# Optimization experiments

Hardware: AMD Instinct MI355X
Metric: run time of the kernel (lower is better)

## Reference

```python
import jax, jax.numpy as jnp
import numpy as np

BIT = 8
QMAX = 2 ** (BIT - 1) - 1          # 127
QMIN = -(2 ** (BIT - 1))           # -128
BOUNDARY_RANGE = 0.005
EPS = 1e-5


def _quant_act_int8(x):
    # StatsQ per-tensor activation quantization: scale from (1 - boundary_range)
    # quantile of |x| (robust absmax), fake-quant with STE.
    amax = jnp.maximum(jnp.quantile(jnp.abs(x), 1.0 - BOUNDARY_RANGE), EPS)
    s = QMAX / amax
    q = jnp.clip(jnp.round(x * s), QMIN, QMAX) / s
    return x + jax.lax.stop_gradient(q - x)


def _quant_w_ternary(w):
    # BitNet-1.58-style per-tensor ternary weight quantization:
    # gamma = mean(|W|); W_q in {-1, 0, +1} * gamma; STE.
    gamma = jnp.mean(jnp.abs(w)) + EPS
    q = jnp.clip(jnp.round(w / gamma), -1.0, 1.0) * gamma
    return w + jax.lax.stop_gradient(q - w)


def _qlinear(x, w):
    # quantize activations (int8 fake-quant) and weights (ternary), then matmul
    xq = _quant_act_int8(x)
    wq = _quant_w_ternary(w)
    return jnp.einsum('btd,hd->bth', xq, wq)


def _layernorm(x, g, b):
    mu = jnp.mean(x, axis=-1, keepdims=True)
    var = jnp.mean(jnp.square(x - mu), axis=-1, keepdims=True)
    return (x - mu) * jax.lax.rsqrt(var + 1e-5) * g + b


def setup_inputs() -> dict:
    key = jax.random.key(0)
    k_x, k_w1, k_w2 = jax.random.split(key, 3)
    B, T, D, H = 64, 256, 1024, 4096
    x = jax.random.normal(k_x, (B, T, D), dtype=jnp.float32)
    ln_g = jnp.ones((D,), dtype=jnp.float32)
    ln_b = jnp.zeros((D,), dtype=jnp.float32)
    w1 = jax.random.normal(k_w1, (H, D), dtype=jnp.float32) * (1.0 / np.sqrt(D))
    w2 = jax.random.normal(k_w2, (D, H), dtype=jnp.float32) * (1.0 / np.sqrt(H))
    return {'x': x, 'ln_g': ln_g, 'ln_b': ln_b, 'w1': w1, 'w2': w2}


def reference(x, ln_g, ln_b, w1, w2):
    h = _layernorm(x, ln_g, ln_b)          # [B,T,D]
    h = _qlinear(h, w1)                    # [B,T,H]
    h = jax.nn.gelu(h, approximate=False)  # torch nn.GELU default = exact erf
    out = _qlinear(h, w2)                  # [B,T,D]
    return out
```

## Files before the change

### kernel.cpp

```cpp
#include <hip/hip_runtime.h>
#include <hip/hip_fp16.h>
#include <math.h>


#define M_ROWS 16384
#define D_DIM  1024
#define H_DIM  4096

typedef int i32x4 __attribute__((ext_vector_type(4)));
typedef int i32x16 __attribute__((ext_vector_type(16)));

#define AS1 __attribute__((address_space(1)))
#define AS3 __attribute__((address_space(3)))

__device__ __forceinline__ void load_lds16(const void* g, void* l) {
  __builtin_amdgcn_global_load_lds((const AS1 void*)g, (AS3 void*)l, 16, 0, 0);
}

__device__ __forceinline__ float block_sum256(float v, float* lds) {
#pragma unroll
  for (int o = 32; o > 0; o >>= 1) v += __shfl_down(v, o, 64);
  int t = threadIdx.x;
  __syncthreads();
  if ((t & 63) == 0) lds[t >> 6] = v;
  __syncthreads();
  return lds[0] + lds[1] + lds[2] + lds[3];
}

__global__ __launch_bounds__(256) void k_layernorm(
    const float* __restrict__ x, const float* __restrict__ g,
    const float* __restrict__ b, __half* __restrict__ out) {
  __shared__ float lds[4];
  int row = blockIdx.x, t = threadIdx.x;
  float4 v = ((const float4*)(x + (size_t)row * D_DIM))[t];
  float s = v.x + v.y + v.z + v.w;
  s = block_sum256(s, lds);
  float mu = s * (1.0f / D_DIM);
  float d0 = v.x - mu, d1 = v.y - mu, d2 = v.z - mu, d3 = v.w - mu;
  float ss = d0 * d0 + d1 * d1 + d2 * d2 + d3 * d3;
  ss = block_sum256(ss, lds);
  float inv = 1.0f / sqrtf(ss * (1.0f / D_DIM) + 1e-5f);
  float4 gg = ((const float4*)g)[t];
  float4 bb = ((const float4*)b)[t];
  __half2 p0 = __floats2half2_rn(d0 * inv * gg.x + bb.x, d1 * inv * gg.y + bb.y);
  __half2 p1 = __floats2half2_rn(d2 * inv * gg.z + bb.z, d3 * inv * gg.w + bb.w);
  uint2 st;
  st.x = *(unsigned*)&p0;
  st.y = *(unsigned*)&p1;
  ((uint2*)(out + (size_t)row * D_DIM))[t] = st;
}

__global__ __launch_bounds__(256) void k_absmean2(const float4* __restrict__ w1,
                                                  const float4* __restrict__ w2,
                                                  size_t n4, double* __restrict__ out) {
  int which = (blockIdx.x >= (gridDim.x >> 1)) ? 1 : 0;
  const float4* p = which ? w2 : w1;
  unsigned half_grid = gridDim.x >> 1;
  unsigned blk = blockIdx.x - which * half_grid;
  double s = 0.0;
  size_t stride = (size_t)half_grid * blockDim.x;
  for (size_t i = (size_t)blk * blockDim.x + threadIdx.x; i < n4; i += stride) {
    float4 v = p[i];
    s += (double)fabsf(v.x) + (double)fabsf(v.y) + (double)fabsf(v.z) + (double)fabsf(v.w);
  }
#pragma unroll
  for (int o = 32; o > 0; o >>= 1) s += __shfl_down(s, o, 64);
  __shared__ double ds[4];
  int t = threadIdx.x;
  if ((t & 63) == 0) ds[t >> 6] = s;
  __syncthreads();
  if (t == 0) atomicAdd(out + which, ds[0] + ds[1] + ds[2] + ds[3]);
}

__device__ __forceinline__ int tern1(float w, float gamma) {
  return (int)fminf(1.f, fmaxf(-1.f, rintf(w / gamma)));
}

__global__ __launch_bounds__(256) void k_wquant2(const float4* __restrict__ w1,
                                                 const float4* __restrict__ w2,
                                                 unsigned* __restrict__ q1,
                                                 unsigned* __restrict__ q2, size_t n4,
                                                 const double* __restrict__ sump,
                                                 double inv_n, float* __restrict__ gamma_out) {
  int which = (blockIdx.x >= (gridDim.x >> 1)) ? 1 : 0;
  const float4* w = which ? w2 : w1;
  unsigned* wq = which ? q2 : q1;
  unsigned half_grid = gridDim.x >> 1;
  unsigned blk = blockIdx.x - which * half_grid;
  float gamma = (float)(sump[which] * inv_n) + 1e-5f;
  if (blk == 0 && threadIdx.x == 0) gamma_out[which] = gamma;
  size_t stride = (size_t)half_grid * blockDim.x;
  for (size_t i = (size_t)blk * blockDim.x + threadIdx.x; i < n4; i += stride) {
    float4 v = w[i];
    int a = tern1(v.x, gamma), b = tern1(v.y, gamma), c = tern1(v.z, gamma), d = tern1(v.w, gamma);
    wq[i] = (unsigned)(a & 255) | ((unsigned)(b & 255) << 8) |
            ((unsigned)(c & 255) << 16) | ((unsigned)(d & 255) << 24);
  }
}

__global__ __launch_bounds__(512) void k_hist16(const uint4* __restrict__ p, size_t n8,
                                                unsigned* __restrict__ hist) {
  extern __shared__ unsigned h[];
  int t = threadIdx.x;
  for (int i = t; i < 32768; i += 512) h[i] = 0;
  __syncthreads();
  size_t stride = (size_t)gridDim.x * 512;
  for (size_t i = (size_t)blockIdx.x * 512 + t; i < n8; i += stride) {
    uint4 u = p[i];
    atomicAdd(&h[u.x & 0x7FFFu], 1u);
    atomicAdd(&h[(u.x >> 16) & 0x7FFFu], 1u);
    atomicAdd(&h[u.y & 0x7FFFu], 1u);
    atomicAdd(&h[(u.y >> 16) & 0x7FFFu], 1u);
    atomicAdd(&h[u.z & 0x7FFFu], 1u);
    atomicAdd(&h[(u.z >> 16) & 0x7FFFu], 1u);
    atomicAdd(&h[u.w & 0x7FFFu], 1u);
    atomicAdd(&h[(u.w >> 16) & 0x7FFFu], 1u);
  }
  __syncthreads();
  for (int i = t; i < 32768; i += 512) {
    unsigned c = h[i];
    if (c) atomicAdd(&hist[i], c);
  }
}

__global__ __launch_bounds__(256) void k_scanq(const unsigned* __restrict__ hist,
                                               float* __restrict__ scl,
                                               unsigned long long k, double frac) {
  __shared__ unsigned tsum[256];
  __shared__ unsigned long long pre[256];
  __shared__ unsigned vk, vk1;
  int t = threadIdx.x;
  unsigned s = 0;
  for (int j = 0; j < 128; ++j) s += hist[t * 128 + j];
  tsum[t] = s;
  __syncthreads();
  if (t == 0) {
    unsigned long long c = 0;
    for (int i = 0; i < 256; ++i) { pre[i] = c; c += tsum[i]; }
  }
  __syncthreads();
  unsigned long long base = pre[t];
  for (int j = 0; j < 128; ++j) {
    unsigned c = hist[t * 128 + j];
    if (base <= k && k < base + c) vk = t * 128 + j;
    if (base <= k + 1 && k + 1 < base + c) vk1 = t * 128 + j;
    base += c;
  }
  __syncthreads();
  if (t == 0) {
    double a = (double)__half2float(__ushort_as_half((unsigned short)vk));
    double b = (double)__half2float(__ushort_as_half((unsigned short)vk1));
    double qv = (frac >= 0.5) ? (b - (b - a) * (1.0 - frac)) : (a + (b - a) * frac);
    float amax = fmaxf((float)qv, 1e-5f);
    scl[0] = amax;
    scl[1] = 127.0f / amax;
  }
}

__device__ __forceinline__ void unpack8(uint4 u, float* f) {
  __half2 h;
  h = *(__half2*)&u.x; f[0] = __low2float(h); f[1] = __high2float(h);
  h = *(__half2*)&u.y; f[2] = __low2float(h); f[3] = __high2float(h);
  h = *(__half2*)&u.z; f[4] = __low2float(h); f[5] = __high2float(h);
  h = *(__half2*)&u.w; f[6] = __low2float(h); f[7] = __high2float(h);
}

__device__ __forceinline__ unsigned qpack4(float a, float b, float c, float d, float s) {
  int qa = (int)fminf(127.f, fmaxf(-128.f, rintf(a * s)));
  int qb = (int)fminf(127.f, fmaxf(-128.f, rintf(b * s)));
  int qc = (int)fminf(127.f, fmaxf(-128.f, rintf(c * s)));
  int qd = (int)fminf(127.f, fmaxf(-128.f, rintf(d * s)));
  return (unsigned)(qa & 255) | ((unsigned)(qb & 255) << 8) |
         ((unsigned)(qc & 255) << 16) | ((unsigned)(qd & 255) << 24);
}

__global__ __launch_bounds__(256) void k_quant16(const uint4* __restrict__ p,
                                                 uint2* __restrict__ q, size_t n8,
                                                 const float* __restrict__ scl) {
  float s = scl[1];
  size_t stride = (size_t)gridDim.x * blockDim.x;
  for (size_t i = (size_t)blockIdx.x * blockDim.x + threadIdx.x; i < n8; i += stride) {
    float f[8];
    unpack8(p[i], f);
    uint2 r;
    r.x = qpack4(f[0], f[1], f[2], f[3], s);
    r.y = qpack4(f[4], f[5], f[6], f[7], s);
    q[i] = r;
  }
}

__device__ __forceinline__ float gelu_fast(float v) {
  float a = fabsf(v) * 0.70710678118654752f;
  float t = __builtin_amdgcn_rcpf(fmaf(0.3275911f, a, 1.0f));
  float p = t * fmaf(t, fmaf(t, fmaf(t, fmaf(t, 1.061405429f, -1.453152027f),
                                     1.421413741f), -0.284496736f), 0.254829592f);
  float e = __expf(-a * a);
  float er = fmaf(-p, e, 1.0f);
  float erf_s = copysignf(er, v);
  return 0.5f * v * (1.0f + erf_s);
}

template <int K, bool GELU>
__global__ __launch_bounds__(512, 2) void k_gemm(const signed char* __restrict__ A,
                                                 const signed char* __restrict__ B,
                                                 int N, void* __restrict__ outp,
                                                 const float* __restrict__ gamma_p,
                                                 const float* __restrict__ scl) {
  constexpr int NT = K / 128;
  extern __shared__ __align__(16) char smem[];
  signed char* As = (signed char*)smem;
  signed char* Bs = (signed char*)smem + 65536;

  const int tid = threadIdx.x;
  const int lane = tid & 63;
  const int wv = tid >> 6;
  const int wr = (wv >> 2) * 128;
  const int wc = (wv & 3) * 64;

  const unsigned nwg = gridDim.x;
  const unsigned q8 = nwg >> 3;
  const unsigned bid = blockIdx.x;
  const unsigned swz = (bid & 7) * q8 + (bid >> 3);
  const unsigned nx = (unsigned)N >> 8;
  const int n0 = (int)(swz % nx) * 256;
  const int m0 = (int)(swz / nx) * 256;

  const signed char* aG[4];
  const signed char* bG[4];
  int sL[4];
#pragma unroll
  for (int j = 0; j < 4; ++j) {
    int g_lin = j * 512 + tid;
    int row = g_lin >> 3;
    int cg = (g_lin & 7) ^ (row & 7);
    aG[j] = A + (size_t)(m0 + row) * K + cg * 16;
    bG[j] = B + (size_t)(n0 + row) * K + cg * 16;
    sL[j] = g_lin * 16;
  }

#define STAGE(t_)                                              \
  {                                                            \
    const size_t ko_ = (size_t)(t_) * 128;                     \
    const int bo_ = ((t_) & 1) << 15;                          \
    _Pragma("unroll") for (int j = 0; j < 4; ++j)              \
        load_lds16(aG[j] + ko_, As + bo_ + sL[j]);             \
    _Pragma("unroll") for (int j = 0; j < 4; ++j)              \
        load_lds16(bG[j] + ko_, Bs + bo_ + sL[j]);             \
  }

  int a_off[4][4], b_off[2][4];
#pragma unroll
  for (int mi = 0; mi < 4; ++mi) {
    int am = wr + mi * 32 + (lane & 31);
#pragma unroll
    for (int p = 0; p < 4; ++p) {
      int g = p * 2 + (lane >> 5);
      a_off[mi][p] = am * 128 + ((g ^ (am & 7)) << 4);
    }
  }
#pragma unroll
  for (int ni = 0; ni < 2; ++ni) {
    int bn = wc + ni * 32 + (lane & 31);
#pragma unroll
    for (int p = 0; p < 4; ++p) {
      int g = p * 2 + (lane >> 5);
      b_off[ni][p] = bn * 128 + ((g ^ (bn & 7)) << 4);
    }
  }

#define RD(fa, fb, bo_, p_)                                      \
  {                                                              \
    _Pragma("unroll") for (int mi = 0; mi < 4; ++mi)             \
        fa[mi] = *(const i32x4*)(As + (bo_) + a_off[mi][p_]);    \
    _Pragma("unroll") for (int ni = 0; ni < 2; ++ni)             \
        fb[ni] = *(const i32x4*)(Bs + (bo_) + b_off[ni][p_]);    \
  }

#define MM(fa, fb)                                                            \
  {                                                                           \
    __builtin_amdgcn_s_setprio(1);                                            \
    _Pragma("unroll") for (int mi = 0; mi < 4; ++mi)                          \
        _Pragma("unroll") for (int ni = 0; ni < 2; ++ni)                      \
            acc[mi][ni] = __builtin_amdgcn_mfma_i32_32x32x32_i8(              \
                fa[mi], fb[ni], acc[mi][ni], 0, 0, 0);                        \
    __builtin_amdgcn_s_setprio(0);                                            \
  }

  i32x16 acc[4][2];
#pragma unroll
  for (int mi = 0; mi < 4; ++mi)
#pragma unroll
    for (int ni = 0; ni < 2; ++ni) acc[mi][ni] = (i32x16)(0);

  i32x4 fA0[4], fB0[2], fA1[4], fB1[2];

  STAGE(0);
  STAGE(1);
  asm volatile("s_waitcnt vmcnt(8)" ::: "memory");
  __builtin_amdgcn_s_barrier();
  RD(fA0, fB0, 0, 0);

#pragma unroll 2
  for (int t = 0; t < NT; ++t) {
    const int bo = (t & 1) << 15;
    if (t >= 1 && t + 1 < NT) STAGE(t + 1);
    RD(fA1, fB1, bo, 1);
    __builtin_amdgcn_sched_barrier(0);
    MM(fA0, fB0);
    __builtin_amdgcn_sched_barrier(0);
    RD(fA0, fB0, bo, 2);
    __builtin_amdgcn_sched_barrier(0);
    MM(fA1, fB1);
    __builtin_amdgcn_sched_barrier(0);
    RD(fA1, fB1, bo, 3);
    __builtin_amdgcn_sched_barrier(0);
    MM(fA0, fB0);
    __builtin_amdgcn_sched_barrier(0);
    MM(fA1, fB1);
    if (t + 1 < NT) {
      asm volatile("s_waitcnt vmcnt(0)" ::: "memory");
      __builtin_amdgcn_s_barrier();
      RD(fA0, fB0, bo ^ 32768, 0);
    }
  }
#undef STAGE
#undef RD
#undef MM

  const float cs = (*gamma_p) / scl[1];
  const int col0 = n0 + wc + (lane & 31);
  const int row0 = m0 + wr + 4 * (lane >> 5);
#pragma unroll
  for (int mi = 0; mi < 4; ++mi) {
#pragma unroll
    for (int ni = 0; ni < 2; ++ni) {
      const int col = col0 + ni * 32;
#pragma unroll
      for (int reg = 0; reg < 16; ++reg) {
        const int row = row0 + mi * 32 + (reg & 3) + 8 * (reg >> 2);
        float v = cs * (float)acc[mi][ni][reg];
        size_t idx = (size_t)row * N + col;
        if (GELU) {
          ((__half*)outp)[idx] = __float2half(gelu_fast(v));
        } else {
          ((float*)outp)[idx] = v;
        }
      }
    }
  }
}

extern "C" void kernel_launch(void* const* d_in, const int* in_sizes, int n_in,
                              void* d_out, int out_size, void* d_ws, size_t ws_size,
                              hipStream_t stream) {
  const float* x = (const float*)d_in[0];
  const float* ln_g = (const float*)d_in[1];
  const float* ln_b = (const float*)d_in[2];
  const float* w1 = (const float*)d_in[3];
  const float* w2 = (const float*)d_in[4];
  float* out = (float*)d_out;

  char* ws = (char*)d_ws;
  __half* h2 = (__half*)ws;
  __half* h1 = (__half*)(ws + ((size_t)128 << 20));
  signed char* xq1 = (signed char*)(ws + ((size_t)160 << 20));
  signed char* xq2 = (signed char*)(ws + ((size_t)128 << 20));
  signed char* w1q = (signed char*)(ws + ((size_t)192 << 20));
  signed char* w2q = (signed char*)(ws + ((size_t)196 << 20));
  char* sm = ws + ((size_t)200 << 20);
  unsigned* hista = (unsigned*)sm;
  unsigned* histb = (unsigned*)(sm + (128 << 10));
  double* wsum = (double*)(sm + (256 << 10));
  float* gamma = (float*)(sm + (256 << 10) + 16);
  float* scl1 = (float*)(sm + (256 << 10) + 32);
  float* scl2 = (float*)(sm + (256 << 10) + 40);

  hipMemsetAsync(sm, 0, (256 << 10) + 64, stream);
  hipFuncSetAttribute((const void*)k_hist16, hipFuncAttributeMaxDynamicSharedMemorySize,
                      131072);
  hipFuncSetAttribute((const void*)(k_gemm<D_DIM, true>),
                      hipFuncAttributeMaxDynamicSharedMemorySize, 131072);
  hipFuncSetAttribute((const void*)(k_gemm<H_DIM, false>),
                      hipFuncAttributeMaxDynamicSharedMemorySize, 131072);

  const double qq = 1.0 - 0.005;
  const unsigned long long N1 = (unsigned long long)M_ROWS * D_DIM;
  const unsigned long long N2 = (unsigned long long)M_ROWS * H_DIM;
  double idx1 = qq * (double)(N1 - 1);
  double idx2 = qq * (double)(N2 - 1);
  unsigned long long k1 = (unsigned long long)idx1;
  unsigned long long k2 = (unsigned long long)idx2;
  double frac1 = idx1 - (double)k1;
  double frac2 = idx2 - (double)k2;

  const size_t nW4 = (size_t)H_DIM * D_DIM / 4;
  const double inv_nW = 1.0 / (double)(H_DIM * D_DIM);

  k_absmean2<<<1024, 256, 0, stream>>>((const float4*)w1, (const float4*)w2, nW4, wsum);
  k_wquant2<<<2048, 256, 0, stream>>>((const float4*)w1, (const float4*)w2,
                                      (unsigned*)w1q, (unsigned*)w2q, nW4, wsum, inv_nW, gamma);

  k_layernorm<<<M_ROWS, 256, 0, stream>>>(x, ln_g, ln_b, h1);

  const size_t n8_1 = N1 / 8;
  k_hist16<<<256, 512, 131072, stream>>>((const uint4*)h1, n8_1, hista);
  k_scanq<<<1, 256, 0, stream>>>(hista, scl1, k1, frac1);
  k_quant16<<<1024, 256, 0, stream>>>((const uint4*)h1, (uint2*)xq1, n8_1, scl1);

  k_gemm<D_DIM, true><<<(H_DIM / 256) * (M_ROWS / 256), 512, 131072, stream>>>(
      xq1, w1q, H_DIM, (void*)h2, gamma + 0, scl1);

  const size_t n8_2 = N2 / 8;
  k_hist16<<<256, 512, 131072, stream>>>((const uint4*)h2, n8_2, histb);
  k_scanq<<<1, 256, 0, stream>>>(histb, scl2, k2, frac2);
  k_quant16<<<2048, 256, 0, stream>>>((const uint4*)h2, (uint2*)xq2, n8_2, scl2);

  k_gemm<H_DIM, false><<<(D_DIM / 256) * (M_ROWS / 256), 512, 131072, stream>>>(
      xq2, w2q, D_DIM, (void*)out, gamma + 1, scl2);
}
```

Measured before the change: 468.2 us.

## Stage GEMM tiles through registers instead of direct global-to-LDS loads

Replaces the direct global_load_lds staging with ordinary global loads into registers, issued two iterations ahead and written to the double-buffered LDS after the compute phases. The explicit fragment ping-pong between LDS reads and MFMA groups is dropped in favour of four simple phases that each read and then multiply. The aim is to overlap global latency with a full tile of MFMA work and to simplify scheduling. The cost is extra VGPRs for the staged tiles, an added barrier per iteration, and less explicit interleaving of LDS reads with MFMAs.

```diff
diff --git a/kernel.cpp b/kernel.cpp
--- a/kernel.cpp
+++ b/kernel.cpp
@@ -9,13 +9,6 @@
 
 typedef int i32x4 __attribute__((ext_vector_type(4)));
 typedef int i32x16 __attribute__((ext_vector_type(16)));
-
-#define AS1 __attribute__((address_space(1)))
-#define AS3 __attribute__((address_space(3)))
-
-__device__ __forceinline__ void load_lds16(const void* g, void* l) {
-  __builtin_amdgcn_global_load_lds((const AS1 void*)g, (AS3 void*)l, 16, 0, 0);
-}
 
 __device__ __forceinline__ float block_sum256(float v, float* lds) {
 #pragma unroll
@@ -225,27 +218,36 @@
   const int n0 = (int)(swz % nx) * 256;
   const int m0 = (int)(swz / nx) * 256;
 
-  const signed char* aG[4];
-  const signed char* bG[4];
-  int sL[4];
+  int aOff[4], bOff[4], sL[4];
 #pragma unroll
   for (int j = 0; j < 4; ++j) {
     int g_lin = j * 512 + tid;
     int row = g_lin >> 3;
     int cg = (g_lin & 7) ^ (row & 7);
-    aG[j] = A + (size_t)(m0 + row) * K + cg * 16;
-    bG[j] = B + (size_t)(n0 + row) * K + cg * 16;
+    aOff[j] = (m0 + row) * K + cg * 16;
+    bOff[j] = (n0 + row) * K + cg * 16;
     sL[j] = g_lin * 16;
   }
 
-#define STAGE(t_)                                              \
-  {                                                            \
-    const size_t ko_ = (size_t)(t_) * 128;                     \
-    const int bo_ = ((t_) & 1) << 15;                          \
-    _Pragma("unroll") for (int j = 0; j < 4; ++j)              \
-        load_lds16(aG[j] + ko_, As + bo_ + sL[j]);             \
-    _Pragma("unroll") for (int j = 0; j < 4; ++j)              \
-        load_lds16(bG[j] + ko_, Bs + bo_ + sL[j]);             \
+  i32x4 rA[4], rB[4];
+
+#define LOADREGS(t_)                                                  \
+  {                                                                   \
+    const int ko_ = (t_) * 128;                                       \
+    _Pragma("unroll") for (int j = 0; j < 4; ++j)                     \
+        rA[j] = *(const i32x4*)(A + (size_t)(aOff[j] + ko_));         \
+    _Pragma("unroll") for (int j = 0; j < 4; ++j)                     \
+        rB[j] = *(const i32x4*)(B + (size_t)(bOff[j] + ko_));         \
+    __builtin_amdgcn_sched_barrier(0);                                \
+  }
+
+#define WRITELDS(t_)                                                  \
+  {                                                                   \
+    const int bo_ = ((t_) & 1) << 15;                                 \
+    _Pragma("unroll") for (int j = 0; j < 4; ++j)                     \
+        *(i32x4*)(As + bo_ + sL[j]) = rA[j];                          \
+    _Pragma("unroll") for (int j = 0; j < 4; ++j)                     \
+        *(i32x4*)(Bs + bo_ + sL[j]) = rB[j];                          \
   }
 
   int a_off[4][4], b_off[2][4];
@@ -268,16 +270,19 @@
     }
   }
 
-#define RD(fa, fb, bo_, p_)                                      \
-  {                                                              \
-    _Pragma("unroll") for (int mi = 0; mi < 4; ++mi)             \
-        fa[mi] = *(const i32x4*)(As + (bo_) + a_off[mi][p_]);    \
-    _Pragma("unroll") for (int ni = 0; ni < 2; ++ni)             \
-        fb[ni] = *(const i32x4*)(Bs + (bo_) + b_off[ni][p_]);    \
-  }
-
-#define MM(fa, fb)                                                            \
+  i32x16 acc[4][2];
+#pragma unroll
+  for (int mi = 0; mi < 4; ++mi)
+#pragma unroll
+    for (int ni = 0; ni < 2; ++ni) acc[mi][ni] = (i32x16)(0);
+
+#define PHASE(bo_, p_)                                                        \
   {                                                                           \
+    i32x4 fa[4], fb[2];                                                       \
+    _Pragma("unroll") for (int mi = 0; mi < 4; ++mi)                          \
+        fa[mi] = *(const i32x4*)(As + (bo_) + a_off[mi][p_]);                 \
+    _Pragma("unroll") for (int ni = 0; ni < 2; ++ni)                          \
+        fb[ni] = *(const i32x4*)(Bs + (bo_) + b_off[ni][p_]);                 \
     __builtin_amdgcn_s_setprio(1);                                            \
     _Pragma("unroll") for (int mi = 0; mi < 4; ++mi)                          \
         _Pragma("unroll") for (int ni = 0; ni < 2; ++ni)                      \
@@ -286,46 +291,31 @@
     __builtin_amdgcn_s_setprio(0);                                            \
   }
 
-  i32x16 acc[4][2];
-#pragma unroll
-  for (int mi = 0; mi < 4; ++mi)
-#pragma unroll
-    for (int ni = 0; ni < 2; ++ni) acc[mi][ni] = (i32x16)(0);
-
-  i32x4 fA0[4], fB0[2], fA1[4], fB1[2];
-
-  STAGE(0);
-  STAGE(1);
-  asm volatile("s_waitcnt vmcnt(8)" ::: "memory");
+  LOADREGS(0);
+  WRITELDS(0);
+  LOADREGS(1);
+  WRITELDS(1);
+  asm volatile("s_waitcnt lgkmcnt(0)" ::: "memory");
   __builtin_amdgcn_s_barrier();
-  RD(fA0, fB0, 0, 0);
 
 #pragma unroll 2
   for (int t = 0; t < NT; ++t) {
     const int bo = (t & 1) << 15;
-    if (t >= 1 && t + 1 < NT) STAGE(t + 1);
-    RD(fA1, fB1, bo, 1);
-    __builtin_amdgcn_sched_barrier(0);
-    MM(fA0, fB0);
-    __builtin_amdgcn_sched_barrier(0);
-    RD(fA0, fB0, bo, 2);
-    __builtin_amdgcn_sched_barrier(0);
-    MM(fA1, fB1);
-    __builtin_amdgcn_sched_barrier(0);
-    RD(fA1, fB1, bo, 3);
-    __builtin_amdgcn_sched_barrier(0);
-    MM(fA0, fB0);
-    __builtin_amdgcn_sched_barrier(0);
-    MM(fA1, fB1);
-    if (t + 1 < NT) {
-      asm volatile("s_waitcnt vmcnt(0)" ::: "memory");
+    if (t + 2 < NT) LOADREGS(t + 2);
+    PHASE(bo, 0);
+    PHASE(bo, 1);
+    PHASE(bo, 2);
+    PHASE(bo, 3);
+    if (t + 2 < NT) {
       __builtin_amdgcn_s_barrier();
-      RD(fA0, fB0, bo ^ 32768, 0);
+      WRITELDS(t + 2);
+      asm volatile("s_waitcnt lgkmcnt(0)" ::: "memory");
+      __builtin_amdgcn_s_barrier();
     }
   }
-#undef STAGE
-#undef RD
-#undef MM
+#undef LOADREGS
+#undef WRITELDS
+#undef PHASE
 
   const float cs = (*gamma_p) / scl[1];
   const int col0 = n0 + wc + (lane & 31);
```

Result: no change. 474.1 us (+1.3%).

## Load GEMM B operand directly into registers, halving LDS footprint

Applied to the files above, without the earlier changes.

The int8 GEMM now stages only the A tile through LDS and has each wave load its B fragments straight from global memory into registers, prefetched one K-tile ahead with double-buffered register sets. Dynamic LDS per block drops from 128KB to 64KB, allowing two blocks per CU and removing B-side LDS reads. The cost is duplicated global reads of B across waves sharing columns, more VGPR pressure, and exposed global latency.

```diff
diff --git a/kernel.cpp b/kernel.cpp
--- a/kernel.cpp
+++ b/kernel.cpp
@@ -209,7 +209,6 @@
   constexpr int NT = K / 128;
   extern __shared__ __align__(16) char smem[];
   signed char* As = (signed char*)smem;
-  signed char* Bs = (signed char*)smem + 65536;
 
   const int tid = threadIdx.x;
   const int lane = tid & 63;
@@ -226,7 +225,6 @@
   const int m0 = (int)(swz / nx) * 256;
 
   const signed char* aG[4];
-  const signed char* bG[4];
   int sL[4];
 #pragma unroll
   for (int j = 0; j < 4; ++j) {
@@ -234,21 +232,30 @@
     int row = g_lin >> 3;
     int cg = (g_lin & 7) ^ (row & 7);
     aG[j] = A + (size_t)(m0 + row) * K + cg * 16;
-    bG[j] = B + (size_t)(n0 + row) * K + cg * 16;
     sL[j] = g_lin * 16;
   }
 
-#define STAGE(t_)                                              \
+#define STAGE_A(t_, DST)                                       \
   {                                                            \
     const size_t ko_ = (size_t)(t_) * 128;                     \
-    const int bo_ = ((t_) & 1) << 15;                          \
     _Pragma("unroll") for (int j = 0; j < 4; ++j)              \
-        load_lds16(aG[j] + ko_, As + bo_ + sL[j]);             \
-    _Pragma("unroll") for (int j = 0; j < 4; ++j)              \
-        load_lds16(bG[j] + ko_, Bs + bo_ + sL[j]);             \
-  }
-
-  int a_off[4][4], b_off[2][4];
+        load_lds16(aG[j] + ko_, As + (DST) + sL[j]);           \
+  }
+
+  const signed char* bP0 = B + (size_t)(n0 + wc + (lane & 31)) * K + ((lane >> 5) << 4);
+  const signed char* bP1 = bP0 + (size_t)32 * K;
+
+  i32x4 bX[8], bY[8];
+
+#define LOAD_B(BN, OFF)                                        \
+  {                                                            \
+    _Pragma("unroll") for (int p = 0; p < 4; ++p)              \
+        BN[p] = *(const i32x4*)(bP0 + (OFF) + p * 32);         \
+    _Pragma("unroll") for (int p = 0; p < 4; ++p)              \
+        BN[4 + p] = *(const i32x4*)(bP1 + (OFF) + p * 32);     \
+  }
+
+  int a_off[4][4];
 #pragma unroll
   for (int mi = 0; mi < 4; ++mi) {
     int am = wr + mi * 32 + (lane & 31);
@@ -258,74 +265,60 @@
       a_off[mi][p] = am * 128 + ((g ^ (am & 7)) << 4);
     }
   }
-#pragma unroll
-  for (int ni = 0; ni < 2; ++ni) {
-    int bn = wc + ni * 32 + (lane & 31);
-#pragma unroll
-    for (int p = 0; p < 4; ++p) {
-      int g = p * 2 + (lane >> 5);
-      b_off[ni][p] = bn * 128 + ((g ^ (bn & 7)) << 4);
-    }
-  }
-
-#define RD(fa, fb, bo_, p_)                                      \
-  {                                                              \
-    _Pragma("unroll") for (int mi = 0; mi < 4; ++mi)             \
-        fa[mi] = *(const i32x4*)(As + (bo_) + a_off[mi][p_]);    \
-    _Pragma("unroll") for (int ni = 0; ni < 2; ++ni)             \
-        fb[ni] = *(const i32x4*)(Bs + (bo_) + b_off[ni][p_]);    \
-  }
-
-#define MM(fa, fb)                                                            \
+
+  i32x16 acc[4][2];
+#pragma unroll
+  for (int mi = 0; mi < 4; ++mi)
+#pragma unroll
+    for (int ni = 0; ni < 2; ++ni) acc[mi][ni] = (i32x16)(0);
+
+#define PHASE(BUF, p_, BC)                                                    \
   {                                                                           \
+    i32x4 fa[4];                                                              \
+    _Pragma("unroll") for (int mi = 0; mi < 4; ++mi)                          \
+        fa[mi] = *(const i32x4*)(As + (BUF) + a_off[mi][p_]);                 \
     __builtin_amdgcn_s_setprio(1);                                            \
     _Pragma("unroll") for (int mi = 0; mi < 4; ++mi)                          \
         _Pragma("unroll") for (int ni = 0; ni < 2; ++ni)                      \
             acc[mi][ni] = __builtin_amdgcn_mfma_i32_32x32x32_i8(              \
-                fa[mi], fb[ni], acc[mi][ni], 0, 0, 0);                        \
+                fa[mi], BC[ni * 4 + p_], acc[mi][ni], 0, 0, 0);               \
     __builtin_amdgcn_s_setprio(0);                                            \
   }
 
-  i32x16 acc[4][2];
-#pragma unroll
-  for (int mi = 0; mi < 4; ++mi)
-#pragma unroll
-    for (int ni = 0; ni < 2; ++ni) acc[mi][ni] = (i32x16)(0);
-
-  i32x4 fA0[4], fB0[2], fA1[4], fB1[2];
-
-  STAGE(0);
-  STAGE(1);
+#define TILE_BODY(tcur, BUF, BCUR, BNXT)                       \
+  {                                                            \
+    if ((tcur) + 1 < NT) {                                     \
+      STAGE_A((tcur) + 1, (BUF) ^ 32768);                      \
+      __builtin_amdgcn_sched_barrier(0);                       \
+      LOAD_B(BNXT, 128);                                       \
+      bP0 += 128; bP1 += 128;                                  \
+    }                                                          \
+    __builtin_amdgcn_sched_barrier(0);                         \
+    PHASE(BUF, 0, BCUR);                                       \
+    PHASE(BUF, 1, BCUR);                                       \
+    PHASE(BUF, 2, BCUR);                                       \
+    PHASE(BUF, 3, BCUR);                                       \
+    if ((tcur) + 1 < NT) {                                     \
+      asm volatile("s_waitcnt vmcnt(8)" ::: "memory");         \
+      __builtin_amdgcn_s_barrier();                            \
+    }                                                          \
+  }
+
+  STAGE_A(0, 0);
+  __builtin_amdgcn_sched_barrier(0);
+  LOAD_B(bX, 0);
   asm volatile("s_waitcnt vmcnt(8)" ::: "memory");
   __builtin_amdgcn_s_barrier();
-  RD(fA0, fB0, 0, 0);
-
-#pragma unroll 2
-  for (int t = 0; t < NT; ++t) {
-    const int bo = (t & 1) << 15;
-    if (t >= 1 && t + 1 < NT) STAGE(t + 1);
-    RD(fA1, fB1, bo, 1);
-    __builtin_amdgcn_sched_barrier(0);
-    MM(fA0, fB0);
-    __builtin_amdgcn_sched_barrier(0);
-    RD(fA0, fB0, bo, 2);
-    __builtin_amdgcn_sched_barrier(0);
-    MM(fA1, fB1);
-    __builtin_amdgcn_sched_barrier(0);
-    RD(fA1, fB1, bo, 3);
-    __builtin_amdgcn_sched_barrier(0);
-    MM(fA0, fB0);
-    __builtin_amdgcn_sched_barrier(0);
-    MM(fA1, fB1);
-    if (t + 1 < NT) {
-      asm volatile("s_waitcnt vmcnt(0)" ::: "memory");
-      __builtin_amdgcn_s_barrier();
-      RD(fA0, fB0, bo ^ 32768, 0);
-    }
-  }
-#undef STAGE
-#undef RD
-#undef MM
+
+#pragma unroll 1
+  for (int t = 0; t < NT; t += 2) {
+    TILE_BODY(t, 0, bX, bY);
+    TILE_BODY(t + 1, 32768, bY, bX);
+  }
+#undef STAGE_A
+#undef LOAD_B
+#undef PHASE
+#undef TILE_BODY
 
   const float cs = (*gamma_p) / scl[1];
   const int col0 = n0 + wc + (lane & 31);
@@ -379,9 +372,9 @@
   hipFuncSetAttribute((const void*)k_hist16, hipFuncAttributeMaxDynamicSharedMemorySize,
                       131072);
   hipFuncSetAttribute((const void*)(k_gemm<D_DIM, true>),
-                      hipFuncAttributeMaxDynamicSharedMemorySize, 131072);
+                      hipFuncAttributeMaxDynamicSharedMemorySize, 65536);
   hipFuncSetAttribute((const void*)(k_gemm<H_DIM, false>),
-                      hipFuncAttributeMaxDynamicSharedMemorySize, 131072);
+                      hipFuncAttributeMaxDynamicSharedMemorySize, 65536);
 
   const double qq = 1.0 - 0.005;
   const unsigned long long N1 = (unsigned long long)M_ROWS * D_DIM;
@@ -407,7 +400,7 @@
   k_scanq<<<1, 256, 0, stream>>>(hista, scl1, k1, frac1);
   k_quant16<<<1024, 256, 0, stream>>>((const uint4*)h1, (uint2*)xq1, n8_1, scl1);
 
-  k_gemm<D_DIM, true><<<(H_DIM / 256) * (M_ROWS / 256), 512, 131072, stream>>>(
+  k_gemm<D_DIM, true><<<(H_DIM / 256) * (M_ROWS / 256), 512, 65536, stream>>>(
       xq1, w1q, H_DIM, (void*)h2, gamma + 0, scl1);
 
   const size_t n8_2 = N2 / 8;
@@ -415,6 +408,6 @@
   k_scanq<<<1, 256, 0, stream>>>(histb, scl2, k2, frac2);
   k_quant16<<<2048, 256, 0, stream>>>((const uint4*)h2, (uint2*)xq2, n8_2, scl2);
 
-  k_gemm<H_DIM, false><<<(D_DIM / 256) * (M_ROWS / 256), 512, 131072, stream>>>(
+  k_gemm<H_DIM, false><<<(D_DIM / 256) * (M_ROWS / 256), 512, 65536, stream>>>(
       xq2, w2q, D_DIM, (void*)out, gamma + 1, scl2);
 }
```

Measured after the change: 522.4 us. 1.12x slower.

## Switch int8 GEMM to triple-buffered 64-wide K stages with interleaved loads

Applied to the files above, without the earlier changes.

The GEMM main loop moves from double-buffered 128-wide K tiles to triple-buffered 64-wide K tiles. It prefetches two stages ahead, splits the global-to-LDS loads into halves interleaved between MFMA groups, and re-derives the LDS XOR swizzle for 64-byte rows. LDS use drops from 128KB to 96KB per block. The aim is to overlap more memory latency with compute and keep MFMA units busy. The cost is extra block-wide barriers per iteration and a non-unrolled loop.

```diff
diff --git a/kernel.cpp b/kernel.cpp
--- a/kernel.cpp
+++ b/kernel.cpp
@@ -206,10 +206,10 @@
                                                  int N, void* __restrict__ outp,
                                                  const float* __restrict__ gamma_p,
                                                  const float* __restrict__ scl) {
-  constexpr int NT = K / 128;
+  constexpr int NT = K / 64;
   extern __shared__ __align__(16) char smem[];
   signed char* As = (signed char*)smem;
-  signed char* Bs = (signed char*)smem + 65536;
+  signed char* Bs = (signed char*)smem + 49152;
 
   const int tid = threadIdx.x;
   const int lane = tid & 63;
@@ -225,106 +225,116 @@
   const int n0 = (int)(swz % nx) * 256;
   const int m0 = (int)(swz / nx) * 256;
 
-  const signed char* aG[4];
-  const signed char* bG[4];
-  int sL[4];
-#pragma unroll
-  for (int j = 0; j < 4; ++j) {
+  const signed char* aG[2];
+  const signed char* bG[2];
+  int sL[2];
+#pragma unroll
+  for (int j = 0; j < 2; ++j) {
     int g_lin = j * 512 + tid;
-    int row = g_lin >> 3;
-    int cg = (g_lin & 7) ^ (row & 7);
+    int row = g_lin >> 2;
+    int cg = (g_lin & 3) ^ ((row >> 1) & 3);
     aG[j] = A + (size_t)(m0 + row) * K + cg * 16;
     bG[j] = B + (size_t)(n0 + row) * K + cg * 16;
     sL[j] = g_lin * 16;
   }
 
-#define STAGE(t_)                                              \
+#define STG(j_, t_, dst_)                                      \
   {                                                            \
-    const size_t ko_ = (size_t)(t_) * 128;                     \
-    const int bo_ = ((t_) & 1) << 15;                          \
-    _Pragma("unroll") for (int j = 0; j < 4; ++j)              \
-        load_lds16(aG[j] + ko_, As + bo_ + sL[j]);             \
-    _Pragma("unroll") for (int j = 0; j < 4; ++j)              \
-        load_lds16(bG[j] + ko_, Bs + bo_ + sL[j]);             \
-  }
-
-  int a_off[4][4], b_off[2][4];
+    const size_t ko_ = (size_t)(t_) * 64;                      \
+    load_lds16(aG[j_] + ko_, As + (dst_) + sL[j_]);            \
+    load_lds16(bG[j_] + ko_, Bs + (dst_) + sL[j_]);            \
+  }
+
+  int a_off[4][2], b_off[2][2];
 #pragma unroll
   for (int mi = 0; mi < 4; ++mi) {
     int am = wr + mi * 32 + (lane & 31);
 #pragma unroll
-    for (int p = 0; p < 4; ++p) {
+    for (int p = 0; p < 2; ++p) {
       int g = p * 2 + (lane >> 5);
-      a_off[mi][p] = am * 128 + ((g ^ (am & 7)) << 4);
+      a_off[mi][p] = am * 64 + ((g ^ ((am >> 1) & 3)) << 4);
     }
   }
 #pragma unroll
   for (int ni = 0; ni < 2; ++ni) {
     int bn = wc + ni * 32 + (lane & 31);
 #pragma unroll
-    for (int p = 0; p < 4; ++p) {
+    for (int p = 0; p < 2; ++p) {
       int g = p * 2 + (lane >> 5);
-      b_off[ni][p] = bn * 128 + ((g ^ (bn & 7)) << 4);
+      b_off[ni][p] = bn * 64 + ((g ^ ((bn >> 1) & 3)) << 4);
     }
   }
 
-#define RD(fa, fb, bo_, p_)                                      \
-  {                                                              \
-    _Pragma("unroll") for (int mi = 0; mi < 4; ++mi)             \
-        fa[mi] = *(const i32x4*)(As + (bo_) + a_off[mi][p_]);    \
-    _Pragma("unroll") for (int ni = 0; ni < 2; ++ni)             \
-        fb[ni] = *(const i32x4*)(Bs + (bo_) + b_off[ni][p_]);    \
-  }
-
-#define MM(fa, fb)                                                            \
+  i32x16 acc[4][2];
+#pragma unroll
+  for (int mi = 0; mi < 4; ++mi)
+#pragma unroll
+    for (int ni = 0; ni < 2; ++ni) acc[mi][ni] = (i32x16)(0);
+
+#define RD_B(bo_)                                              \
+  {                                                            \
+    fb[0] = *(const i32x4*)(Bs + (bo_) + b_off[0][0]);         \
+    fb[1] = *(const i32x4*)(Bs + (bo_) + b_off[0][1]);         \
+    fb[2] = *(const i32x4*)(Bs + (bo_) + b_off[1][0]);         \
+    fb[3] = *(const i32x4*)(Bs + (bo_) + b_off[1][1]);         \
+  }
+#define RD_A(bo_, ma_, mb_)                                    \
+  {                                                            \
+    fa[0] = *(const i32x4*)(As + (bo_) + a_off[ma_][0]);       \
+    fa[1] = *(const i32x4*)(As + (bo_) + a_off[ma_][1]);       \
+    fa[2] = *(const i32x4*)(As + (bo_) + a_off[mb_][0]);       \
+    fa[3] = *(const i32x4*)(As + (bo_) + a_off[mb_][1]);       \
+  }
+#define MM(ma_, mb_)                                                          \
   {                                                                           \
     __builtin_amdgcn_s_setprio(1);                                            \
-    _Pragma("unroll") for (int mi = 0; mi < 4; ++mi)                          \
-        _Pragma("unroll") for (int ni = 0; ni < 2; ++ni)                      \
-            acc[mi][ni] = __builtin_amdgcn_mfma_i32_32x32x32_i8(              \
-                fa[mi], fb[ni], acc[mi][ni], 0, 0, 0);                        \
+    acc[ma_][0] = __builtin_amdgcn_mfma_i32_32x32x32_i8(fa[0], fb[0], acc[ma_][0], 0, 0, 0); \
+    acc[ma_][1] = __builtin_amdgcn_mfma_i32_32x32x32_i8(fa[0], fb[2], acc[ma_][1], 0, 0, 0); \
+    acc[mb_][0] = __builtin_amdgcn_mfma_i32_32x32x32_i8(fa[2], fb[0], acc[mb_][0], 0, 0, 0); \
+    acc[mb_][1] = __builtin_amdgcn_mfma_i32_32x32x32_i8(fa[2], fb[2], acc[mb_][1], 0, 0, 0); \
+    acc[ma_][0] = __builtin_amdgcn_mfma_i32_32x32x32_i8(fa[1], fb[1], acc[ma_][0], 0, 0, 0); \
+    acc[ma_][1] = __builtin_amdgcn_mfma_i32_32x32x32_i8(fa[1], fb[3], acc[ma_][1], 0, 0, 0); \
+    acc[mb_][0] = __builtin_amdgcn_mfma_i32_32x32x32_i8(fa[3], fb[1], acc[mb_][0], 0, 0, 0); \
+    acc[mb_][1] = __builtin_amdgcn_mfma_i32_32x32x32_i8(fa[3], fb[3], acc[mb_][1], 0, 0, 0); \
     __builtin_amdgcn_s_setprio(0);                                            \
   }
 
-  i32x16 acc[4][2];
-#pragma unroll
-  for (int mi = 0; mi < 4; ++mi)
-#pragma unroll
-    for (int ni = 0; ni < 2; ++ni) acc[mi][ni] = (i32x16)(0);
-
-  i32x4 fA0[4], fB0[2], fA1[4], fB1[2];
-
-  STAGE(0);
-  STAGE(1);
-  asm volatile("s_waitcnt vmcnt(8)" ::: "memory");
+  STG(0, 0, 0);
+  STG(1, 0, 0);
+  STG(0, 1, 16384);
+  STG(1, 1, 16384);
+  asm volatile("s_waitcnt vmcnt(4)" ::: "memory");
   __builtin_amdgcn_s_barrier();
-  RD(fA0, fB0, 0, 0);
-
-#pragma unroll 2
+
+#pragma unroll 1
   for (int t = 0; t < NT; ++t) {
-    const int bo = (t & 1) << 15;
-    if (t >= 1 && t + 1 < NT) STAGE(t + 1);
-    RD(fA1, fB1, bo, 1);
+    const int bo = (t % 3) * 16384;
+    const int bo2 = ((t + 2) % 3) * 16384;
+    const bool st = (t + 2 < NT);
+    i32x4 fa[4], fb[4];
+    RD_B(bo);
+    RD_A(bo, 0, 1);
+    if (st) STG(0, t + 2, bo2);
     __builtin_amdgcn_sched_barrier(0);
-    MM(fA0, fB0);
+    __builtin_amdgcn_s_barrier();
+    MM(0, 1);
     __builtin_amdgcn_sched_barrier(0);
-    RD(fA0, fB0, bo, 2);
+    __builtin_amdgcn_s_barrier();
+    RD_A(bo, 2, 3);
+    if (st) STG(1, t + 2, bo2);
     __builtin_amdgcn_sched_barrier(0);
-    MM(fA1, fB1);
+    __builtin_amdgcn_s_barrier();
+    MM(2, 3);
     __builtin_amdgcn_sched_barrier(0);
-    RD(fA1, fB1, bo, 3);
-    __builtin_amdgcn_sched_barrier(0);
-    MM(fA0, fB0);
-    __builtin_amdgcn_sched_barrier(0);
-    MM(fA1, fB1);
     if (t + 1 < NT) {
-      asm volatile("s_waitcnt vmcnt(0)" ::: "memory");
+      if (st) { asm volatile("s_waitcnt vmcnt(4)" ::: "memory"); }
+      else    { asm volatile("s_waitcnt vmcnt(0)" ::: "memory"); }
       __builtin_amdgcn_s_barrier();
-      RD(fA0, fB0, bo ^ 32768, 0);
     }
   }
-#undef STAGE
-#undef RD
+#undef STG
+#undef RD_B
+#undef RD_A
 #undef MM
 
   const float cs = (*gamma_p) / scl[1];
@@ -379,9 +389,9 @@
   hipFuncSetAttribute((const void*)k_hist16, hipFuncAttributeMaxDynamicSharedMemorySize,
                       131072);
   hipFuncSetAttribute((const void*)(k_gemm<D_DIM, true>),
-                      hipFuncAttributeMaxDynamicSharedMemorySize, 131072);
+                      hipFuncAttributeMaxDynamicSharedMemorySize, 98304);
   hipFuncSetAttribute((const void*)(k_gemm<H_DIM, false>),
-                      hipFuncAttributeMaxDynamicSharedMemorySize, 131072);
+                      hipFuncAttributeMaxDynamicSharedMemorySize, 98304);
 
   const double qq = 1.0 - 0.005;
   const unsigned long long N1 = (unsigned long long)M_ROWS * D_DIM;
@@ -407,7 +417,7 @@
   k_scanq<<<1, 256, 0, stream>>>(hista, scl1, k1, frac1);
   k_quant16<<<1024, 256, 0, stream>>>((const uint4*)h1, (uint2*)xq1, n8_1, scl1);
 
-  k_gemm<D_DIM, true><<<(H_DIM / 256) * (M_ROWS / 256), 512, 131072, stream>>>(
+  k_gemm<D_DIM, true><<<(H_DIM / 256) * (M_ROWS / 256), 512, 98304, stream>>>(
       xq1, w1q, H_DIM, (void*)h2, gamma + 0, scl1);
 
   const size_t n8_2 = N2 / 8;
@@ -415,6 +425,6 @@
   k_scanq<<<1, 256, 0, stream>>>(histb, scl2, k2, frac2);
   k_quant16<<<2048, 256, 0, stream>>>((const uint4*)h2, (uint2*)xq2, n8_2, scl2);
 
-  k_gemm<H_DIM, false><<<(D_DIM / 256) * (M_ROWS / 256), 512, 131072, stream>>>(
+  k_gemm<H_DIM, false><<<(D_DIM / 256) * (M_ROWS / 256), 512, 98304, stream>>>(
       xq2, w2q, D_DIM, (void*)out, gamma + 1, scl2);
 }
```

Result: slower. 486.4 us (+3.9%).
